# Performance work log

Hardware: AMD Instinct MI355X
Metric: run time of the kernel (lower is better)

The kernel has to match this reference:

```python
import jax, jax.numpy as jnp
import numpy as np

DIM_HEAD = 64
LN_EPS = 1e-6  # flax nn.LayerNorm default


def setup_inputs() -> dict:
    key = jax.random.key(0)
    ks = jax.random.split(key, 5)
    B, N, D, H, Dh = 4, 1024, 768, 12, 64
    x = jax.random.normal(ks[0], (B, N, D), dtype=jnp.float32)
    Wq = jax.random.normal(ks[1], (D, H, Dh), dtype=jnp.float32) * (1.0 / np.sqrt(D))
    Wk = jax.random.normal(ks[2], (D, H, Dh), dtype=jnp.float32) * (1.0 / np.sqrt(D))
    Wv = jax.random.normal(ks[3], (D, H, Dh), dtype=jnp.float32) * (1.0 / np.sqrt(D))
    theta = jax.random.normal(ks[4], (H, H), dtype=jnp.float32) * (1.0 / np.sqrt(H))
    ln_scale = jnp.ones((N,), dtype=jnp.float32)
    ln_bias = jnp.zeros((N,), dtype=jnp.float32)
    return {"x": x, "Wq": Wq, "Wk": Wk, "Wv": Wv, "theta": theta,
            "ln_scale": ln_scale, "ln_bias": ln_bias}


def reference(x, Wq, Wk, Wv, theta, ln_scale, ln_bias):
    # x: [B, N, D]; W*: [D, H, Dh]; theta: [H, H]; ln_*: [N]
    q = jnp.einsum('bnd,dhe->bnhe', x, Wq) / jnp.sqrt(jnp.float32(DIM_HEAD))
    k = jnp.einsum('bnd,dhe->bnhe', x, Wk)
    v = jnp.einsum('bnd,dhe->bnhe', x, Wv)
    # attention scores over key axis: [B, H, N, N]
    attn = jnp.einsum('bqhd,bkhd->bhqk', q, k)
    attn = jax.nn.softmax(attn, axis=-1)
    # cross-head theta mixing: 'h i, b h q k -> b i q k'
    attn = jnp.einsum('hi,bhqk->biqk', theta, attn)
    # LayerNorm over last (key) axis with learnable scale/bias of shape [N]
    mean = jnp.mean(attn, axis=-1, keepdims=True)
    var = jnp.mean(jnp.square(attn - mean), axis=-1, keepdims=True)
    attn = (attn - mean) * jax.lax.rsqrt(var + LN_EPS) * ln_scale + ln_bias
    # note: output indexed by k (as in the original source einsum)
    out = jnp.einsum('bhqk,bqhd->bkhd', attn, v)
    B, N, H, Dh = out.shape
    return out.reshape(B, N, H * Dh)
```

## Files before the change

kernel.cpp:

```cpp
#include <hip/hip_runtime.h>

#define NB    4
#define NSEQ  1024
#define DMODEL 768
#define NH    12
#define DH    64

typedef __bf16 bf16x8 __attribute__((ext_vector_type(8)));
typedef float  floatx4 __attribute__((ext_vector_type(4)));
typedef unsigned int u32;

static __device__ __forceinline__ float bf2f(unsigned short u) {
    return __uint_as_float(((unsigned)u) << 16);
}
static __device__ __forceinline__ unsigned short f2bf(float f) {
    unsigned u = __float_as_uint(f);
    u += 0x7FFFu + ((u >> 16) & 1u);
    return (unsigned short)(u >> 16);
}

static __device__ __forceinline__ void gl_lds16(const void* g, void* l) {
    __builtin_amdgcn_global_load_lds(
        (const __attribute__((address_space(1))) unsigned int*)g,
        (__attribute__((address_space(3))) unsigned int*)l, 16, 0, 0);
}

__global__ __launch_bounds__(256) void cast_x(
    const float* __restrict__ x, unsigned short* __restrict__ xb)
{
    const int g = blockIdx.x * 256 + threadIdx.x;
    const size_t base = (size_t)g * 8;
    float4 a = *(const float4*)(x + base);
    float4 b = *(const float4*)(x + base + 4);
    unsigned short o[8];
    o[0] = f2bf(a.x); o[1] = f2bf(a.y); o[2] = f2bf(a.z); o[3] = f2bf(a.w);
    o[4] = f2bf(b.x); o[5] = f2bf(b.y); o[6] = f2bf(b.z); o[7] = f2bf(b.w);
    *(uint4*)(xb + base) = *(uint4*)o;
}

__global__ __launch_bounds__(256) void tr_w(
    const float* __restrict__ Wq, const float* __restrict__ Wk,
    const float* __restrict__ Wv, unsigned short* __restrict__ Wt)
{
    const int z  = blockIdx.z;
    const float* __restrict__ W = (z == 0) ? Wq : (z == 1) ? Wk : Wv;
    const int c0 = blockIdx.x * 64;
    const int k0 = blockIdx.y * 64;
    const int t  = threadIdx.x;

    __shared__ float ls[64][65];

    const int lr = t >> 2;
    #pragma unroll
    for (int j = 0; j < 4; j++) {
        int col = (t & 3) * 16 + j * 4;
        float4 v = *(const float4*)(W + (size_t)(k0 + lr) * DMODEL + c0 + col);
        ls[lr][col + 0] = v.x; ls[lr][col + 1] = v.y;
        ls[lr][col + 2] = v.z; ls[lr][col + 3] = v.w;
    }
    __syncthreads();
    const int lc = t >> 2;
    #pragma unroll
    for (int j = 0; j < 4; j++) {
        int kb = (t & 3) * 16 + j * 4;
        ushort4 o;
        o.x = f2bf(ls[kb + 0][lc]); o.y = f2bf(ls[kb + 1][lc]);
        o.z = f2bf(ls[kb + 2][lc]); o.w = f2bf(ls[kb + 3][lc]);
        *(ushort4*)(Wt + (size_t)z * DMODEL * DMODEL + (size_t)(c0 + lc) * DMODEL + k0 + kb) = o;
    }
}

__global__ __launch_bounds__(256) void qkv_mfma(
    const unsigned short* __restrict__ xb, const unsigned short* __restrict__ Wt,
    unsigned short* __restrict__ Q, unsigned short* __restrict__ K,
    unsigned short* __restrict__ V)
{
    const int z  = blockIdx.z;
    const int r0 = blockIdx.x * 64;
    const int c0 = blockIdx.y * 128;
    const int t    = threadIdx.x;
    const int wave = t >> 6, lane = t & 63;
    const int m = lane & 15, g = lane >> 4;

    const unsigned short* __restrict__ B = Wt + (size_t)z * DMODEL * DMODEL;

    __shared__ __align__(16) char sm[17408];
    unsigned short (*As)[32] = (unsigned short(*)[32])sm;
    unsigned short (*Bs)[32] = (unsigned short(*)[32])(sm + 4096);
    unsigned short (*Po)[136] = (unsigned short(*)[136])sm;

    const int wm = (wave >> 1) * 32;
    const int wn = (wave & 1) * 64;

    floatx4 acc[2][4] = {};

    const unsigned short* ga  = xb + (size_t)(r0 + (t >> 2)) * DMODEL + (t & 3) * 8;
    const unsigned short* gb0 = B  + (size_t)(c0 + (t >> 2)) * DMODEL + (t & 3) * 8;
    const unsigned short* gb1 = B  + (size_t)(c0 + 64 + (t >> 2)) * DMODEL + (t & 3) * 8;
    unsigned short* la  = (unsigned short*)sm + (size_t)t * 8;
    unsigned short* lb0 = (unsigned short*)(sm + 4096) + (size_t)t * 8;
    unsigned short* lb1 = (unsigned short*)(sm + 4096) + (size_t)(t + 256) * 8;

    for (int kk = 0; kk < DMODEL / 32; kk++) {
        gl_lds16(ga  + kk * 32, la);
        gl_lds16(gb0 + kk * 32, lb0);
        gl_lds16(gb1 + kk * 32, lb1);
        __syncthreads();

        bf16x8 af[2], bf[4];
        #pragma unroll
        for (int mt = 0; mt < 2; mt++)
            af[mt] = *(const bf16x8*)&As[wm + mt * 16 + m][g * 8];
        #pragma unroll
        for (int nt = 0; nt < 4; nt++)
            bf[nt] = *(const bf16x8*)&Bs[wn + nt * 16 + m][g * 8];
        #pragma unroll
        for (int mt = 0; mt < 2; mt++)
            #pragma unroll
            for (int nt = 0; nt < 4; nt++)
                acc[mt][nt] = __builtin_amdgcn_mfma_f32_16x16x32_bf16(
                    af[mt], bf[nt], acc[mt][nt], 0, 0, 0);
        __syncthreads();
    }

    const float scale = (z == 0) ? 0.125f : 1.0f;
    #pragma unroll
    for (int mt = 0; mt < 2; mt++) {
        #pragma unroll
        for (int nt = 0; nt < 4; nt++) {
            int rloc = wm + mt * 16 + g * 4;
            int cloc = wn + nt * 16 + m;
            #pragma unroll
            for (int r = 0; r < 4; r++)
                Po[rloc + r][cloc] = f2bf(acc[mt][nt][r] * scale);
        }
    }
    __syncthreads();

    #pragma unroll
    for (int i = 0; i < 4; i++) {
        int ci = t + i * 256;
        int row = ci >> 4, off = (ci & 15) * 8;
        uint4 val = *(uint4*)&Po[row][off];
        if (z == 0) {
            *(uint4*)(Q + (size_t)(r0 + row) * DMODEL + c0 + off) = val;
        } else {
            unsigned short* P = (z == 1) ? K : V;
            int rr = r0 + row;
            int b = rr >> 10, n = rr & 1023;
            int cc = c0 + off;
            int h = cc >> 6, d = cc & 63;
            *(uint4*)(P + (((size_t)b * NH + h) * NSEQ + n) * DH + d) = val;
        }
    }
}

__global__ __launch_bounds__(256) void score_gemm(
    const unsigned short* __restrict__ Q, const unsigned short* __restrict__ K,
    unsigned short* __restrict__ P, float* __restrict__ Lpart)
{
    const int bh = blockIdx.z;
    const int b  = bh / NH, h = bh % NH;
    const int q0 = blockIdx.x * 128;
    const int k0 = blockIdx.y * 128;
    const int t    = threadIdx.x;
    const int wave = t >> 6, lane = t & 63;

    __shared__ __align__(16) char sm[36864];
    unsigned short (*Qs)[72] = (unsigned short(*)[72])sm;
    unsigned short (*Ks)[72] = (unsigned short(*)[72])(sm + 18432);
    unsigned short (*Po)[136] = (unsigned short(*)[136])sm;
    float (*rsum)[2] = (float(*)[2])(sm + 34816);

    #pragma unroll
    for (int i = 0; i < 4; i++) {
        int c = t + i * 256;
        int row = c >> 3, off = (c & 7) * 8;
        uint4 qa = *(const uint4*)(Q + ((size_t)(b * NSEQ + q0 + row)) * DMODEL + h * DH + off);
        uint4 ka = *(const uint4*)(K + (((size_t)bh) * NSEQ + (k0 + row)) * DH + off);
        *(uint4*)&Qs[row][off] = qa;
        *(uint4*)&Ks[row][off] = ka;
    }
    __syncthreads();

    const int wq = (wave >> 1) * 64, wk2 = (wave & 1) * 64;
    const int m = lane & 15, g = lane >> 4;

    floatx4 acc[4][4] = {};
    #pragma unroll
    for (int ds = 0; ds < 2; ds++) {
        const int dd = ds * 32 + g * 8;
        bf16x8 af[4], bf[4];
        #pragma unroll
        for (int mt = 0; mt < 4; mt++)
            af[mt] = *(const bf16x8*)&Qs[wq + mt * 16 + m][dd];
        #pragma unroll
        for (int nt = 0; nt < 4; nt++)
            bf[nt] = *(const bf16x8*)&Ks[wk2 + nt * 16 + m][dd];
        #pragma unroll
        for (int mt = 0; mt < 4; mt++)
            #pragma unroll
            for (int nt = 0; nt < 4; nt++)
                acc[mt][nt] = __builtin_amdgcn_mfma_f32_16x16x32_bf16(
                    af[mt], bf[nt], acc[mt][nt], 0, 0, 0);
    }

    __syncthreads();
    float rs[4][4] = {};
    #pragma unroll
    for (int mt = 0; mt < 4; mt++) {
        #pragma unroll
        for (int nt = 0; nt < 4; nt++) {
            int qloc = wq + mt * 16 + g * 4;
            int kloc = wk2 + nt * 16 + m;
            #pragma unroll
            for (int r = 0; r < 4; r++) {
                float e = __expf(acc[mt][nt][r]);
                Po[qloc + r][kloc] = f2bf(e);
                rs[mt][r] += e;
            }
        }
    }
    #pragma unroll
    for (int mt = 0; mt < 4; mt++)
        #pragma unroll
        for (int r = 0; r < 4; r++) {
            float x = rs[mt][r];
            #pragma unroll
            for (int off = 1; off < 16; off <<= 1)
                x += __shfl_xor(x, off, 64);
            rs[mt][r] = x;
        }
    if (m == 0) {
        #pragma unroll
        for (int mt = 0; mt < 4; mt++)
            #pragma unroll
            for (int r = 0; r < 4; r++)
                rsum[wq + mt * 16 + g * 4 + r][wk2 >> 6] = rs[mt][r];
    }
    __syncthreads();

    if (t < 128)
        Lpart[((size_t)bh * 8 + blockIdx.y) * NSEQ + q0 + t] = rsum[t][0] + rsum[t][1];

    #pragma unroll
    for (int i = 0; i < 8; i++) {
        int c = t + i * 256;
        int row = c >> 4, off = (c & 15) * 8;
        *(uint4*)(P + (((size_t)bh * NSEQ) + q0 + row) * NSEQ + k0 + off) =
            *(uint4*)&Po[row][off];
    }
}

static __device__ __forceinline__ void reduce12(
    const float* v, float* out12, float* red, int t)
{
    const int lane = t & 63, w = t >> 6;
    #pragma unroll
    for (int h = 0; h < 12; h++) {
        float x = v[h];
        #pragma unroll
        for (int off = 32; off > 0; off >>= 1)
            x += __shfl_down(x, off, 64);
        if (lane == 0) red[w * 12 + h] = x;
    }
    __syncthreads();
    if (t < 12) {
        float x = red[t];
        #pragma unroll
        for (int w2 = 1; w2 < 4; w2++) x += red[w2 * 12 + t];
        out12[t] = x;
    }
    __syncthreads();
}

__global__ __launch_bounds__(256) void mix_t(
    unsigned short* __restrict__ P, const float* __restrict__ theta,
    const float* __restrict__ Lpart, float* __restrict__ Rbuf)
{
    const int q = blockIdx.x, b = blockIdx.y, t = threadIdx.x;
    __shared__ float th_s[144], red[48], l_s2[12], l_mean[12];

    if (t < 12) {
        float s = 0.f;
        #pragma unroll
        for (int kt = 0; kt < 8; kt++)
            s += Lpart[(((size_t)(b * NH + t)) * 8 + kt) * NSEQ + q];
        red[36 + t] = s;
        float mean = 0.f;
        #pragma unroll
        for (int h = 0; h < 12; h++) mean += theta[h * 12 + t];
        l_mean[t] = mean * (1.0f / 1024.0f);
    }
    __syncthreads();
    if (t < 144) th_s[t] = theta[t] * (1.0f / red[36 + t / 12]);
    __syncthreads();

    unsigned short* Pq = P + ((size_t)b * NH * NSEQ + q) * NSEQ;
    const int k0 = 4 * t;

    float p[12][4];
    #pragma unroll
    for (int h = 0; h < NH; h++) {
        ushort4 u = *(const ushort4*)(Pq + (size_t)h * NSEQ * NSEQ + k0);
        p[h][0] = bf2f(u.x); p[h][1] = bf2f(u.y);
        p[h][2] = bf2f(u.z); p[h][3] = bf2f(u.w);
    }

    float sT2[12];
    #pragma unroll
    for (int i = 0; i < 12; i++) {
        float s0 = 0.f, s1 = 0.f, s2 = 0.f, s3 = 0.f;
        #pragma unroll
        for (int h = 0; h < 12; h++) {
            float th = th_s[h * 12 + i];
            s0 = fmaf(th, p[h][0], s0); s1 = fmaf(th, p[h][1], s1);
            s2 = fmaf(th, p[h][2], s2); s3 = fmaf(th, p[h][3], s3);
        }
        ushort4 o;
        o.x = f2bf(s0); o.y = f2bf(s1); o.z = f2bf(s2); o.w = f2bf(s3);
        *(ushort4*)(Pq + (size_t)i * NSEQ * NSEQ + k0) = o;
        sT2[i] = fmaf(s0, s0, fmaf(s1, s1, fmaf(s2, s2, s3 * s3)));
    }
    reduce12(sT2, l_s2, red, t);
    if (t < 12) {
        float mean = l_mean[t];
        float var  = l_s2[t] * (1.0f / 1024.0f) - mean * mean;
        Rbuf[(b * NH + t) * NSEQ + q] = rsqrtf(var + 1e-6f);
    }
}

__global__ __launch_bounds__(256) void av_mfma(
    const unsigned short* __restrict__ A, const unsigned short* __restrict__ V,
    const float* __restrict__ Rbuf, const float* __restrict__ theta,
    const float* __restrict__ ln_scale, const float* __restrict__ ln_bias,
    float* __restrict__ out)
{
    const int b  = blockIdx.z;
    const int i  = blockIdx.y;
    const int k0 = blockIdx.x * 64;
    const int t  = threadIdx.x;
    const int wave = t >> 6, lane = t & 63;
    const int m = lane & 15, g = lane >> 4;

    __shared__ __align__(16) u32 At[64 * 33 + 64];
    __shared__ __align__(16) u32 Vt[64 * 33 + 64];

    const unsigned short* Ai = A + ((size_t)(b * NH + i)) * NSEQ * NSEQ;
    const unsigned short* Vi = V + ((size_t)(b * NH + i)) * NSEQ * DH;
    const float* Rb = Rbuf + (size_t)(b * NH + i) * NSEQ;

    const int wk = (wave >> 1) * 32;
    const int wd = (wave & 1) * 32;

    floatx4 acc[2][2] = {};
    float c1[4] = {}, c2[4] = {};
    const int k4s = (t & 15) * 4;

    for (int q0 = 0; q0 < NSEQ; q0 += 64) {
        ushort4 a0[2], a1[2], v0[2], v1[2];
        float2 rr[2];
        #pragma unroll
        for (int l = 0; l < 2; l++) {
            int c = t + l * 256;
            int k4 = (c & 15) * 4;
            int qp = c >> 4;
            a0[l] = *(const ushort4*)(Ai + (size_t)(q0 + 2 * qp)     * NSEQ + k0 + k4);
            a1[l] = *(const ushort4*)(Ai + (size_t)(q0 + 2 * qp + 1) * NSEQ + k0 + k4);
            v0[l] = *(const ushort4*)(Vi + (size_t)(q0 + 2 * qp)     * DH + k4);
            v1[l] = *(const ushort4*)(Vi + (size_t)(q0 + 2 * qp + 1) * DH + k4);
            rr[l] = *(const float2*)(Rb + q0 + 2 * qp);
        }
        __syncthreads();
        #pragma unroll
        for (int l = 0; l < 2; l++) {
            int c = t + l * 256;
            int k4 = (c & 15) * 4;
            int qp = c >> 4;
            const unsigned short* pa0 = (const unsigned short*)&a0[l];
            const unsigned short* pa1 = (const unsigned short*)&a1[l];
            const unsigned short* pv0 = (const unsigned short*)&v0[l];
            const unsigned short* pv1 = (const unsigned short*)&v1[l];
            #pragma unroll
            for (int j = 0; j < 4; j++) {
                At[(k4 + j) * 33 + qp] = (u32)pa0[j] | ((u32)pa1[j] << 16);
                float vf0 = bf2f(pv0[j]), vf1 = bf2f(pv1[j]);
                float s0 = rr[l].x * vf0, s1 = rr[l].y * vf1;
                Vt[(k4 + j) * 33 + qp] = (u32)f2bf(s0) | ((u32)f2bf(s1) << 16);
                c1[j] += s0 + s1;
                c2[j] += vf0 + vf1;
            }
        }
        __syncthreads();

        #pragma unroll
        for (int ks = 0; ks < 2; ks++) {
            const int qo = ks * 16 + g * 4;
            bf16x8 af[2], bf[2];
            #pragma unroll
            for (int mt = 0; mt < 2; mt++) {
                const u32* r = &At[(wk + mt * 16 + m) * 33 + qo];
                uint4 w; w.x = r[0]; w.y = r[1]; w.z = r[2]; w.w = r[3];
                af[mt] = *(bf16x8*)&w;
            }
            #pragma unroll
            for (int nt = 0; nt < 2; nt++) {
                const u32* r = &Vt[(wd + nt * 16 + m) * 33 + qo];
                uint4 w; w.x = r[0]; w.y = r[1]; w.z = r[2]; w.w = r[3];
                bf[nt] = *(bf16x8*)&w;
            }
            #pragma unroll
            for (int mt = 0; mt < 2; mt++)
                #pragma unroll
                for (int nt = 0; nt < 2; nt++)
                    acc[mt][nt] = __builtin_amdgcn_mfma_f32_16x16x32_bf16(
                        af[mt], bf[nt], acc[mt][nt], 0, 0, 0);
        }
    }

    __syncthreads();
    float* c1l = (float*)At;
    float* c2l = (float*)Vt;
    const int grp = t >> 4;
    #pragma unroll
    for (int j = 0; j < 4; j++) {
        c1l[grp * 64 + k4s + j] = c1[j];
        c2l[grp * 64 + k4s + j] = c2[j];
    }
    __syncthreads();
    if (t < 64) {
        float s1_ = 0.f, s2_ = 0.f;
        #pragma unroll
        for (int g2 = 0; g2 < 16; g2++) {
            s1_ += c1l[g2 * 64 + t];
            s2_ += c2l[g2 * 64 + t];
        }
        c1l[1024 + t] = s1_;
        c2l[1024 + t] = s2_;
    }
    __syncthreads();

    float mean = 0.f;
    #pragma unroll
    for (int h = 0; h < 12; h++) mean += theta[h * 12 + i];
    mean *= (1.0f / 1024.0f);

    #pragma unroll
    for (int mt = 0; mt < 2; mt++) {
        int kb = k0 + wk + mt * 16 + g * 4;
        float4 ls4 = *(const float4*)(ln_scale + kb);
        float4 lb4 = *(const float4*)(ln_bias + kb);
        #pragma unroll
        for (int nt = 0; nt < 2; nt++) {
            int d = wd + nt * 16 + m;
            float C1d = c1l[1024 + d], C2d = c2l[1024 + d];
            #pragma unroll
            for (int r = 0; r < 4; r++) {
                float lns = (&ls4.x)[r], lnb = (&lb4.x)[r];
                float val = lns * (acc[mt][nt][r] - mean * C1d) + lnb * C2d;
                out[((size_t)(b * NSEQ + kb + r)) * DMODEL + i * DH + d] = val;
            }
        }
    }
}

extern "C" void kernel_launch(void* const* d_in, const int* in_sizes, int n_in,
                              void* d_out, int out_size, void* d_ws, size_t ws_size,
                              hipStream_t stream) {
    const float* x     = (const float*)d_in[0];
    const float* Wq    = (const float*)d_in[1];
    const float* Wk    = (const float*)d_in[2];
    const float* Wv    = (const float*)d_in[3];
    const float* theta = (const float*)d_in[4];
    const float* ln_s  = (const float*)d_in[5];
    const float* ln_b  = (const float*)d_in[6];
    float* out = (float*)d_out;

    char* ws = (char*)d_ws;
    const size_t qsz = (size_t)NB * NSEQ * DMODEL * sizeof(unsigned short);
    unsigned short* Q = (unsigned short*)(ws);
    unsigned short* K = (unsigned short*)(ws + qsz);
    unsigned short* V = (unsigned short*)(ws + 2 * qsz);
    unsigned short* P = (unsigned short*)(ws + 3 * qsz);
    unsigned short* xb = P;
    unsigned short* Wt = P + (size_t)NB * NSEQ * DMODEL;

    float* Lpart = out;
    float* Rbuf  = (float*)K;

    cast_x<<<dim3(NB * NSEQ * DMODEL / 2048), 256, 0, stream>>>(x, xb);
    tr_w<<<dim3(12, 12, 3), 256, 0, stream>>>(Wq, Wk, Wv, Wt);
    qkv_mfma<<<dim3(NB * NSEQ / 64, DMODEL / 128, 3), 256, 0, stream>>>(
        xb, Wt, Q, K, V);
    score_gemm<<<dim3(NSEQ / 128, NSEQ / 128, NB * NH), 256, 0, stream>>>(Q, K, P, Lpart);
    mix_t<<<dim3(NSEQ, NB), 256, 0, stream>>>(P, theta, Lpart, Rbuf);
    av_mfma<<<dim3(NSEQ / 64, NH, NB), 256, 0, stream>>>(
        P, V, Rbuf, theta, ln_s, ln_b, out);
}
```

Measured before the change: 217.2 us.

## Enlarge QKV GEMM row tile and restructure theta-mix to one wave per query

The QKV projection GEMM now computes 128x128 tiles instead of 64x128, so each wave holds a 4x4 grid of MFMA accumulators and each loaded B tile is reused across more rows. The theta-mixing kernel now gives each wave one query row and loops over four key chunks. Row-sum normalisation and the sum of squares are reduced with wave shuffles, which removes the shared-memory reductions and block barriers. The cost is more registers and LDS per GEMM block, fewer GEMM blocks, theta read from global memory inside the inner loop, and a serial loop of four chunks per wave.

After: 230.3 us. +6.0%, slower.

```diff
diff --git a/kernel.cpp b/kernel.cpp
--- a/kernel.cpp
+++ b/kernel.cpp
@@ -76,7 +76,7 @@
     unsigned short* __restrict__ V)
 {
     const int z  = blockIdx.z;
-    const int r0 = blockIdx.x * 64;
+    const int r0 = blockIdx.x * 128;
     const int c0 = blockIdx.y * 128;
     const int t    = threadIdx.x;
     const int wave = t >> 6, lane = t & 63;
@@ -84,38 +84,41 @@
 
     const unsigned short* __restrict__ B = Wt + (size_t)z * DMODEL * DMODEL;
 
-    __shared__ __align__(16) char sm[17408];
+    __shared__ __align__(16) char sm[34816];
     unsigned short (*As)[32] = (unsigned short(*)[32])sm;
-    unsigned short (*Bs)[32] = (unsigned short(*)[32])(sm + 4096);
+    unsigned short (*Bs)[32] = (unsigned short(*)[32])(sm + 8192);
     unsigned short (*Po)[136] = (unsigned short(*)[136])sm;
 
-    const int wm = (wave >> 1) * 32;
+    const int wm = (wave >> 1) * 64;
     const int wn = (wave & 1) * 64;
 
-    floatx4 acc[2][4] = {};
-
-    const unsigned short* ga  = xb + (size_t)(r0 + (t >> 2)) * DMODEL + (t & 3) * 8;
+    floatx4 acc[4][4] = {};
+
+    const unsigned short* ga0 = xb + (size_t)(r0 + (t >> 2)) * DMODEL + (t & 3) * 8;
+    const unsigned short* ga1 = ga0 + (size_t)64 * DMODEL;
     const unsigned short* gb0 = B  + (size_t)(c0 + (t >> 2)) * DMODEL + (t & 3) * 8;
-    const unsigned short* gb1 = B  + (size_t)(c0 + 64 + (t >> 2)) * DMODEL + (t & 3) * 8;
-    unsigned short* la  = (unsigned short*)sm + (size_t)t * 8;
-    unsigned short* lb0 = (unsigned short*)(sm + 4096) + (size_t)t * 8;
-    unsigned short* lb1 = (unsigned short*)(sm + 4096) + (size_t)(t + 256) * 8;
+    const unsigned short* gb1 = gb0 + (size_t)64 * DMODEL;
+    unsigned short* la0 = (unsigned short*)sm + (size_t)t * 8;
+    unsigned short* la1 = la0 + 2048;
+    unsigned short* lb0 = (unsigned short*)(sm + 8192) + (size_t)t * 8;
+    unsigned short* lb1 = lb0 + 2048;
 
     for (int kk = 0; kk < DMODEL / 32; kk++) {
-        gl_lds16(ga  + kk * 32, la);
+        gl_lds16(ga0 + kk * 32, la0);
+        gl_lds16(ga1 + kk * 32, la1);
         gl_lds16(gb0 + kk * 32, lb0);
         gl_lds16(gb1 + kk * 32, lb1);
         __syncthreads();
 
-        bf16x8 af[2], bf[4];
-        #pragma unroll
-        for (int mt = 0; mt < 2; mt++)
+        bf16x8 af[4], bf[4];
+        #pragma unroll
+        for (int mt = 0; mt < 4; mt++)
             af[mt] = *(const bf16x8*)&As[wm + mt * 16 + m][g * 8];
         #pragma unroll
         for (int nt = 0; nt < 4; nt++)
             bf[nt] = *(const bf16x8*)&Bs[wn + nt * 16 + m][g * 8];
         #pragma unroll
-        for (int mt = 0; mt < 2; mt++)
+        for (int mt = 0; mt < 4; mt++)
             #pragma unroll
             for (int nt = 0; nt < 4; nt++)
                 acc[mt][nt] = __builtin_amdgcn_mfma_f32_16x16x32_bf16(
@@ -125,7 +128,7 @@
 
     const float scale = (z == 0) ? 0.125f : 1.0f;
     #pragma unroll
-    for (int mt = 0; mt < 2; mt++) {
+    for (int mt = 0; mt < 4; mt++) {
         #pragma unroll
         for (int nt = 0; nt < 4; nt++) {
             int rloc = wm + mt * 16 + g * 4;
@@ -138,19 +141,19 @@
     __syncthreads();
 
     #pragma unroll
-    for (int i = 0; i < 4; i++) {
+    for (int i = 0; i < 8; i++) {
         int ci = t + i * 256;
         int row = ci >> 4, off = (ci & 15) * 8;
         uint4 val = *(uint4*)&Po[row][off];
         if (z == 0) {
             *(uint4*)(Q + (size_t)(r0 + row) * DMODEL + c0 + off) = val;
         } else {
-            unsigned short* P = (z == 1) ? K : V;
+            unsigned short* Pp = (z == 1) ? K : V;
             int rr = r0 + row;
-            int b = rr >> 10, n = rr & 1023;
+            int bb = rr >> 10, n = rr & 1023;
             int cc = c0 + off;
             int h = cc >> 6, d = cc & 63;
-            *(uint4*)(P + (((size_t)b * NH + h) * NSEQ + n) * DH + d) = val;
+            *(uint4*)(Pp + (((size_t)bb * NH + h) * NSEQ + n) * DH + d) = val;
         }
     }
 }
@@ -252,81 +255,77 @@
     }
 }
 
-static __device__ __forceinline__ void reduce12(
-    const float* v, float* out12, float* red, int t)
-{
-    const int lane = t & 63, w = t >> 6;
-    #pragma unroll
-    for (int h = 0; h < 12; h++) {
-        float x = v[h];
-        #pragma unroll
-        for (int off = 32; off > 0; off >>= 1)
-            x += __shfl_down(x, off, 64);
-        if (lane == 0) red[w * 12 + h] = x;
-    }
-    __syncthreads();
-    if (t < 12) {
-        float x = red[t];
-        #pragma unroll
-        for (int w2 = 1; w2 < 4; w2++) x += red[w2 * 12 + t];
-        out12[t] = x;
-    }
-    __syncthreads();
-}
-
 __global__ __launch_bounds__(256) void mix_t(
     unsigned short* __restrict__ P, const float* __restrict__ theta,
     const float* __restrict__ Lpart, float* __restrict__ Rbuf)
 {
-    const int q = blockIdx.x, b = blockIdx.y, t = threadIdx.x;
-    __shared__ float th_s[144], red[48], l_s2[12], l_mean[12];
-
-    if (t < 12) {
+    const int t = threadIdx.x;
+    const int wave = t >> 6, lane = t & 63;
+    const int b = blockIdx.y;
+    const int q = blockIdx.x * 4 + wave;
+
+    float rl = 0.f;
+    float mean = 0.f;
+    if (lane < 12) {
         float s = 0.f;
         #pragma unroll
         for (int kt = 0; kt < 8; kt++)
-            s += Lpart[(((size_t)(b * NH + t)) * 8 + kt) * NSEQ + q];
-        red[36 + t] = s;
-        float mean = 0.f;
-        #pragma unroll
-        for (int h = 0; h < 12; h++) mean += theta[h * 12 + t];
-        l_mean[t] = mean * (1.0f / 1024.0f);
-    }
-    __syncthreads();
-    if (t < 144) th_s[t] = theta[t] * (1.0f / red[36 + t / 12]);
-    __syncthreads();
+            s += Lpart[(((size_t)(b * NH + lane)) * 8 + kt) * NSEQ + q];
+        rl = 1.0f / s;
+        #pragma unroll
+        for (int h = 0; h < 12; h++) mean += theta[h * 12 + lane];
+        mean *= (1.0f / 1024.0f);
+    }
+    float rlv[12];
+    #pragma unroll
+    for (int h = 0; h < 12; h++) rlv[h] = __shfl(rl, h, 64);
 
     unsigned short* Pq = P + ((size_t)b * NH * NSEQ + q) * NSEQ;
-    const int k0 = 4 * t;
-
-    float p[12][4];
-    #pragma unroll
-    for (int h = 0; h < NH; h++) {
-        ushort4 u = *(const ushort4*)(Pq + (size_t)h * NSEQ * NSEQ + k0);
-        p[h][0] = bf2f(u.x); p[h][1] = bf2f(u.y);
-        p[h][2] = bf2f(u.z); p[h][3] = bf2f(u.w);
-    }
-
-    float sT2[12];
+    float rs[12] = {};
+
+    #pragma unroll 1
+    for (int kc = 0; kc < 4; kc++) {
+        const int k0 = kc * 256 + lane * 4;
+        float p[12][4];
+        #pragma unroll
+        for (int h = 0; h < 12; h++) {
+            ushort4 u = *(const ushort4*)(Pq + (size_t)h * NSEQ * NSEQ + k0);
+            p[h][0] = bf2f(u.x) * rlv[h];
+            p[h][1] = bf2f(u.y) * rlv[h];
+            p[h][2] = bf2f(u.z) * rlv[h];
+            p[h][3] = bf2f(u.w) * rlv[h];
+        }
+        #pragma unroll
+        for (int i = 0; i < 12; i++) {
+            float s0 = 0.f, s1 = 0.f, s2 = 0.f, s3 = 0.f;
+            #pragma unroll
+            for (int h = 0; h < 12; h++) {
+                float th = theta[h * 12 + i];
+                s0 = fmaf(th, p[h][0], s0); s1 = fmaf(th, p[h][1], s1);
+                s2 = fmaf(th, p[h][2], s2); s3 = fmaf(th, p[h][3], s3);
+            }
+            ushort4 o;
+            o.x = f2bf(s0); o.y = f2bf(s1); o.z = f2bf(s2); o.w = f2bf(s3);
+            *(ushort4*)(Pq + (size_t)i * NSEQ * NSEQ + k0) = o;
+            rs[i] += fmaf(s0, s0, fmaf(s1, s1, fmaf(s2, s2, s3 * s3)));
+        }
+    }
+
     #pragma unroll
     for (int i = 0; i < 12; i++) {
-        float s0 = 0.f, s1 = 0.f, s2 = 0.f, s3 = 0.f;
-        #pragma unroll
-        for (int h = 0; h < 12; h++) {
-            float th = th_s[h * 12 + i];
-            s0 = fmaf(th, p[h][0], s0); s1 = fmaf(th, p[h][1], s1);
-            s2 = fmaf(th, p[h][2], s2); s3 = fmaf(th, p[h][3], s3);
-        }
-        ushort4 o;
-        o.x = f2bf(s0); o.y = f2bf(s1); o.z = f2bf(s2); o.w = f2bf(s3);
-        *(ushort4*)(Pq + (size_t)i * NSEQ * NSEQ + k0) = o;
-        sT2[i] = fmaf(s0, s0, fmaf(s1, s1, fmaf(s2, s2, s3 * s3)));
-    }
-    reduce12(sT2, l_s2, red, t);
-    if (t < 12) {
-        float mean = l_mean[t];
-        float var  = l_s2[t] * (1.0f / 1024.0f) - mean * mean;
-        Rbuf[(b * NH + t) * NSEQ + q] = rsqrtf(var + 1e-6f);
+        float x = rs[i];
+        #pragma unroll
+        for (int off = 32; off > 0; off >>= 1)
+            x += __shfl_xor(x, off, 64);
+        rs[i] = x;
+    }
+    float myrs = 0.f;
+    #pragma unroll
+    for (int i = 0; i < 12; i++)
+        if (lane == i) myrs = rs[i];
+    if (lane < 12) {
+        float var = myrs * (1.0f / 1024.0f) - mean * mean;
+        Rbuf[(size_t)(b * NH + lane) * NSEQ + q] = rsqrtf(var + 1e-6f);
     }
 }
 
@@ -490,10 +489,10 @@
 
     cast_x<<<dim3(NB * NSEQ * DMODEL / 2048), 256, 0, stream>>>(x, xb);
     tr_w<<<dim3(12, 12, 3), 256, 0, stream>>>(Wq, Wk, Wv, Wt);
-    qkv_mfma<<<dim3(NB * NSEQ / 64, DMODEL / 128, 3), 256, 0, stream>>>(
+    qkv_mfma<<<dim3(NB * NSEQ / 128, DMODEL / 128, 3), 256, 0, stream>>>(
         xb, Wt, Q, K, V);
     score_gemm<<<dim3(NSEQ / 128, NSEQ / 128, NB * NH), 256, 0, stream>>>(Q, K, P, Lpart);
-    mix_t<<<dim3(NSEQ, NB), 256, 0, stream>>>(P, theta, Lpart, Rbuf);
+    mix_t<<<dim3(NSEQ / 4, NB), 256, 0, stream>>>(P, theta, Lpart, Rbuf);
     av_mfma<<<dim3(NSEQ / 64, NH, NB), 256, 0, stream>>>(
         P, V, Rbuf, theta, ln_s, ln_b, out);
 }
```
